# Kernel optimization log

Measured on AMD Instinct MI355X. Metric: run time of the kernel, lower is better.

## Reference

```python
import jax, jax.numpy as jnp
import numpy as np

D_MODEL = 1024
NUM_HEADS = 16
HEAD_DIM = D_MODEL // NUM_HEADS  # 64
SEQ = 2048
BATCH = 4
LN_EPS = 1e-5


def setup_inputs() -> dict:
    key = jax.random.key(0)
    k_in, k_qkv, k_o, k_g = jax.random.split(key, 4)
    inputs = jax.random.normal(k_in, (BATCH, SEQ, D_MODEL), dtype=jnp.float32)
    mask = jnp.zeros((BATCH, 1, SEQ, SEQ), dtype=jnp.float32)  # additive mask
    # Realistic rotary embeddings (RoPE), duplicated-halves layout
    inv_freq = 1.0 / (10000.0 ** (jnp.arange(0, HEAD_DIM, 2, dtype=jnp.float32) / HEAD_DIM))
    pos = jnp.arange(SEQ, dtype=jnp.float32)
    freqs = pos[:, None] * inv_freq[None, :]            # [S, Dh/2]
    emb = jnp.concatenate([freqs, freqs], axis=-1)       # [S, Dh]
    cos = jnp.cos(emb)
    sin = jnp.sin(emb)
    # Parameters
    sd = 1.0 / np.sqrt(D_MODEL)
    w_qkv = jax.random.normal(k_qkv, (D_MODEL, 3 * D_MODEL), dtype=jnp.float32) * sd
    w_o = jax.random.normal(k_o, (D_MODEL, D_MODEL), dtype=jnp.float32) * sd
    ln_gamma = jnp.ones((D_MODEL,), dtype=jnp.float32)
    return {"inputs": inputs, "mask": mask, "cos": cos, "sin": sin,
            "ln_gamma": ln_gamma, "w_qkv": w_qkv, "w_o": w_o}


def _rotate_half(x):
    x1, x2 = jnp.split(x, 2, axis=-1)
    return jnp.concatenate([-x2, x1], axis=-1)


def reference(inputs, mask, cos, sin, ln_gamma, w_qkv, w_o):
    B, S, D = inputs.shape
    # Pre-attention LayerNorm (layer_id != 0), center=False -> no beta
    mu = jnp.mean(inputs, axis=-1, keepdims=True)
    var = jnp.mean(jnp.square(inputs - mu), axis=-1, keepdims=True)
    x = (inputs - mu) / jnp.sqrt(var + LN_EPS) * ln_gamma
    # Fused QKV projection, split into heads: [B, H, S, Dh]
    qkv = (x @ w_qkv).reshape(B, S, 3, NUM_HEADS, HEAD_DIM)
    qkv = jnp.transpose(qkv, (2, 0, 3, 1, 4))
    q, k, v = qkv[0], qkv[1], qkv[2]
    # RoPE
    c = cos.reshape(1, 1, S, HEAD_DIM)
    s = sin.reshape(1, 1, S, HEAD_DIM)
    q = q * c + _rotate_half(q) * s
    k = k * c + _rotate_half(k) * s
    # Scaled dot-product attention with additive mask
    scale = 1.0 / jnp.sqrt(jnp.asarray(HEAD_DIM, dtype=q.dtype))
    logits = jnp.einsum("bhqd,bhkd->bhqk", q, k) * scale + mask
    attn = jax.nn.softmax(logits, axis=-1)
    out = jnp.einsum("bhqk,bhkd->bhqd", attn, v)
    out = jnp.transpose(out, (0, 2, 1, 3)).reshape(B, S, D)
    return out @ w_o
```

## Files before the change

kernel.cpp:

```cpp
#include <hip/hip_runtime.h>
#include <stdint.h>

#define DEV __device__ __forceinline__

typedef __bf16 bf16x8 __attribute__((ext_vector_type(8)));
typedef float f32x4 __attribute__((ext_vector_type(4)));
typedef float f32x16 __attribute__((ext_vector_type(16)));

DEV unsigned short f2bf(float f) {
  union { float f; uint32_t u; } c; c.f = f;
  uint32_t u = c.u;
  u += 0x7FFFu + ((u >> 16) & 1u);
  return (unsigned short)(u >> 16);
}
DEV float bf2f(unsigned short h) {
  union { uint32_t u; float f; } c; c.u = ((uint32_t)h) << 16;
  return c.f;
}
DEV float u2f(uint32_t u) {
  union { uint32_t u; float f; } c; c.u = u;
  return c.f;
}
DEV bf16x8 ld8(const unsigned short* p) {
  uint4 u = *reinterpret_cast<const uint4*>(p);
  return __builtin_bit_cast(bf16x8, u);
}
DEV uint32_t cvtpk(float lo, float hi) {
  uint32_t r;
  asm("v_cvt_pk_bf16_f32 %0, %1, %2" : "=v"(r) : "v"(lo), "v"(hi));
  return r;
}
DEV void permswap(uint32_t& a, uint32_t& b) {
  asm("v_permlane32_swap_b32 %0, %1" : "+v"(a), "+v"(b));
}
DEV float exp2b(float x) { return __builtin_amdgcn_exp2f(x); }
DEV void gload16(const void* g, void* l) {
  __builtin_amdgcn_global_load_lds((const __attribute__((address_space(1))) void*)g,
                                   (__attribute__((address_space(3))) void*)l, 16, 0, 0);
}

template<int K, int N>
__global__ __launch_bounds__(256)
void transpose_cast_kernel(const float* __restrict__ in, unsigned short* __restrict__ out) {
  __shared__ float tile[64][65];
  const int bk = blockIdx.x % (K / 64);
  const int bn = blockIdx.x / (K / 64);
  const int k0 = bk * 64, n0 = bn * 64;
  const int t = threadIdx.x;
#pragma unroll
  for (int i = 0; i < 16; ++i) {
    int idx = t + i * 256;
    int kl = idx >> 6, nl = idx & 63;
    tile[kl][nl] = in[(size_t)(k0 + kl) * N + n0 + nl];
  }
  __syncthreads();
#pragma unroll
  for (int i = 0; i < 16; ++i) {
    int idx = t + i * 256;
    int nl = idx >> 6, kl = idx & 63;
    out[(size_t)(n0 + nl) * K + k0 + kl] = f2bf(tile[kl][nl]);
  }
}

__global__ __launch_bounds__(256)
void ln_kernel(const float* __restrict__ x, const float* __restrict__ gamma,
               unsigned short* __restrict__ y) {
  const int row = blockIdx.x;
  const int t = threadIdx.x;
  const float4 v = reinterpret_cast<const float4*>(x + (size_t)row * 1024)[t];
  float s  = v.x + v.y + v.z + v.w;
  float s2 = v.x * v.x + v.y * v.y + v.z * v.z + v.w * v.w;
#pragma unroll
  for (int off = 1; off < 64; off <<= 1) {
    s  += __shfl_xor(s, off);
    s2 += __shfl_xor(s2, off);
  }
  __shared__ float red[8];
  const int w = t >> 6, lane = t & 63;
  if (lane == 0) { red[w] = s; red[4 + w] = s2; }
  __syncthreads();
  s  = red[0] + red[1] + red[2] + red[3];
  s2 = red[4] + red[5] + red[6] + red[7];
  const float mu = s * (1.0f / 1024.0f);
  const float var = s2 * (1.0f / 1024.0f) - mu * mu;
  const float rstd = rsqrtf(var + 1e-5f);
  const float4 g = reinterpret_cast<const float4*>(gamma)[t];
  ushort4 o;
  o.x = f2bf((v.x - mu) * rstd * g.x);
  o.y = f2bf((v.y - mu) * rstd * g.y);
  o.z = f2bf((v.z - mu) * rstd * g.z);
  o.w = f2bf((v.w - mu) * rstd * g.w);
  reinterpret_cast<ushort4*>(y + (size_t)row * 1024)[t] = o;
}

template<int N_DIM, bool OUT_F32>
__global__ __launch_bounds__(256)
void gemm_bt_kernel(const unsigned short* __restrict__ A,
                    const unsigned short* __restrict__ Bt,
                    void* __restrict__ Cout) {
  constexpr int K = 1024;
  __shared__ unsigned short a_lds[128 * 32];
  __shared__ unsigned short b_lds[128 * 32];
  const int t = threadIdx.x;
  const int w = t >> 6, l = t & 63;
  const int lrow = l & 15, lch = l >> 4;
  const int nbn = N_DIM / 128;
  const int m0 = (blockIdx.x / nbn) * 128;
  const int n0 = (blockIdx.x % nbn) * 128;
  const int wm = (w >> 1) * 64, wn = (w & 1) * 64;

  const int srow = t >> 2;
  const int schk = t & 3;
  const int scol = ((schk ^ (srow & 3)) << 3);
  const unsigned short* aS0 = A  + (size_t)(m0 + srow) * K + scol;
  const unsigned short* aS1 = A  + (size_t)(m0 + 64 + srow) * K + scol;
  const unsigned short* bS0 = Bt + (size_t)(n0 + srow) * K + scol;
  const unsigned short* bS1 = Bt + (size_t)(n0 + 64 + srow) * K + scol;
  unsigned short* aD0 = a_lds + (w * 16) * 32;
  unsigned short* aD1 = a_lds + (64 + w * 16) * 32;
  unsigned short* bD0 = b_lds + (w * 16) * 32;
  unsigned short* bD1 = b_lds + (64 + w * 16) * 32;

  f32x4 acc[4][4] = {};

  for (int k0 = 0; k0 < K; k0 += 32) {
    gload16(aS0 + k0, aD0);
    gload16(aS1 + k0, aD1);
    gload16(bS0 + k0, bD0);
    gload16(bS1 + k0, bD1);
    __syncthreads();
    bf16x8 af[4], bfr[4];
#pragma unroll
    for (int m = 0; m < 4; ++m) {
      int row = wm + m * 16 + lrow;
      af[m] = ld8(a_lds + row * 32 + ((lch ^ (lrow & 3)) << 3));
    }
#pragma unroll
    for (int n = 0; n < 4; ++n) {
      int row = wn + n * 16 + lrow;
      bfr[n] = ld8(b_lds + row * 32 + ((lch ^ (lrow & 3)) << 3));
    }
#pragma unroll
    for (int m = 0; m < 4; ++m)
#pragma unroll
      for (int n = 0; n < 4; ++n)
        acc[m][n] = __builtin_amdgcn_mfma_f32_16x16x32_bf16(af[m], bfr[n], acc[m][n], 0, 0, 0);
    __syncthreads();
  }

#pragma unroll
  for (int m = 0; m < 4; ++m) {
    const int grow0 = m0 + wm + m * 16 + lch * 4;
#pragma unroll
    for (int n = 0; n < 4; ++n) {
      const int gcol = n0 + wn + n * 16 + lrow;
#pragma unroll
      for (int r = 0; r < 4; ++r) {
        if constexpr (OUT_F32)
          ((float*)Cout)[(size_t)(grow0 + r) * N_DIM + gcol] = acc[m][n][r];
        else
          ((unsigned short*)Cout)[(size_t)(grow0 + r) * N_DIM + gcol] = f2bf(acc[m][n][r]);
      }
    }
  }
}

__global__ __launch_bounds__(256)
void rope_split_kernel(const unsigned short* __restrict__ qkv,
                       const float* __restrict__ cosb,
                       const float* __restrict__ sinb,
                       unsigned short* __restrict__ Qo,
                       unsigned short* __restrict__ Ko,
                       unsigned short* __restrict__ Vo) {
  const int bid = blockIdx.x;
  const int sb = bid & 31, h = (bid >> 5) & 15, b = bid >> 9;
  const int s0 = sb * 64;
  const int t = threadIdx.x;
  __shared__ unsigned short qt[64][72], kt[64][72], vt[64][72];

  const int sl = t >> 2, c0 = (t & 3) * 16;
  {
    const size_t base = (size_t)(b * 2048 + s0 + sl) * 3072 + h * 64 + c0;
    uint4 q1 = *(const uint4*)(qkv + base);
    uint4 q2 = *(const uint4*)(qkv + base + 8);
    uint4 k1 = *(const uint4*)(qkv + base + 1024);
    uint4 k2 = *(const uint4*)(qkv + base + 1032);
    uint4 v1 = *(const uint4*)(qkv + base + 2048);
    uint4 v2 = *(const uint4*)(qkv + base + 2056);
    *(uint4*)&qt[sl][c0] = q1; *(uint4*)&qt[sl][c0 + 8] = q2;
    *(uint4*)&kt[sl][c0] = k1; *(uint4*)&kt[sl][c0 + 8] = k2;
    *(uint4*)&vt[sl][c0] = v1; *(uint4*)&vt[sl][c0 + 8] = v2;
  }
  __syncthreads();
  {
    const int sg = s0 + sl;
    alignas(16) unsigned short qo16[16], ko16[16];
#pragma unroll
    for (int j = 0; j < 16; ++j) {
      const int d = c0 + j;
      const float cv = cosb[sg * 64 + d], sv = sinb[sg * 64 + d];
      const float qv = bf2f(qt[sl][d]), qp = bf2f(qt[sl][d ^ 32]);
      const float kv = bf2f(kt[sl][d]), kp = bf2f(kt[sl][d ^ 32]);
      const float rq = qv * cv + ((d < 32) ? -qp : qp) * sv;
      const float rk = kv * cv + ((d < 32) ? -kp : kp) * sv;
      qo16[j] = f2bf(rq * 0.180336880f);
      ko16[j] = f2bf(rk);
    }
    const size_t ob = ((size_t)(b * 16 + h) * 2048 + sg) * 64 + c0;
    *(uint4*)(Qo + ob) = *(uint4*)qo16; *(uint4*)(Qo + ob + 8) = *(uint4*)(qo16 + 8);
    *(uint4*)(Ko + ob) = *(uint4*)ko16; *(uint4*)(Ko + ob + 8) = *(uint4*)(ko16 + 8);
  }
  {
    const int dh = t >> 2, sc0 = (t & 3) * 16;
    alignas(16) unsigned short vo16[16];
#pragma unroll
    for (int j = 0; j < 16; ++j) vo16[j] = vt[sc0 + j][dh];
    const size_t ob = ((size_t)(b * 16 + h) * 64 + dh) * 2048 + s0 + sc0;
    *(uint4*)(Vo + ob) = *(uint4*)vo16; *(uint4*)(Vo + ob + 8) = *(uint4*)(vo16 + 8);
  }
}

__global__ __launch_bounds__(256)
void mask_flags_kernel(const float* __restrict__ mask, unsigned char* __restrict__ flg) {
  const int bid = blockIdx.x;
  const int kvt = bid & 31, qc = (bid >> 5) & 31, b = bid >> 10;
  const int t = threadIdx.x;
  uint32_t orbits = 0;
  const int r = t >> 2, c0 = (t & 3) * 16;
  const float* src = mask + (size_t)b * (2048ull * 2048) + (size_t)(qc * 64 + r) * 2048 + kvt * 64 + c0;
#pragma unroll
  for (int i = 0; i < 4; ++i) {
    const float4 v = *(const float4*)(src + i * 4);
    orbits |= __float_as_uint(v.x) | __float_as_uint(v.y) |
              __float_as_uint(v.z) | __float_as_uint(v.w);
  }
  const int nz = __syncthreads_or(orbits != 0u);
  if (t == 0) flg[(size_t)(b * 32 + kvt) * 32 + qc] = (unsigned char)(nz != 0);
}

__global__ __launch_bounds__(256)
void mask_retile_kernel(const float* __restrict__ mask, unsigned short* __restrict__ mrs,
                        const unsigned char* __restrict__ flg) {
  const int bid = blockIdx.x;
  const int kvt = bid & 31, qc = (bid >> 5) & 31, b = bid >> 10;
  if (!flg[(size_t)(b * 32 + kvt) * 32 + qc]) return;
  const int t = threadIdx.x;
  __shared__ float tile[64][72];
  {
    const int r = t >> 2, c0 = (t & 3) * 16;
    const float* src = mask + (size_t)b * (2048ull * 2048) + (size_t)(qc * 64 + r) * 2048 + kvt * 64 + c0;
#pragma unroll
    for (int i = 0; i < 4; ++i) {
      const float4 v = *(const float4*)(src + i * 4);
      *(float4*)&tile[r][c0 + i * 4] = v;
    }
  }
  __syncthreads();
  const int cid = t >> 5;
  const int n = cid >> 2, jj = (cid >> 1) & 1, hi = cid & 1;
  const int qq0 = (t & 31) * 2;
  const int cb = n * 32 + jj * 16 + hi * 4;
  unsigned short* dst = mrs + (((size_t)(b * 32 + kvt) * 8 + cid) * 2048 + qc * 64) * 8;
#pragma unroll
  for (int qo = 0; qo < 2; ++qo) {
    const int q = qq0 + qo;
    alignas(16) unsigned short o8[8];
#pragma unroll
    for (int v = 0; v < 8; ++v) {
      const int col = cb + (v >> 2) * 8 + (v & 3);
      o8[v] = f2bf(tile[q][col] * 1.44269504f);
    }
    *(uint4*)(dst + (size_t)q * 8) = *(uint4*)o8;
  }
}

__global__ __launch_bounds__(256)
void attn_kernel(const unsigned short* __restrict__ Q,
                 const unsigned short* __restrict__ Kg,
                 const unsigned short* __restrict__ Vt,
                 const unsigned short* __restrict__ mrs,
                 const unsigned char* __restrict__ flg,
                 unsigned short* __restrict__ O) {
  const int t = threadIdx.x, w = t >> 6, l = t & 63;
  const int lq = l & 31, hi = l >> 5;
  const int bid = blockIdx.x;
  const int x = bid & 7, y = bid >> 3;
  const int bh = x * 8 + (y & 7), qb = y >> 3;
  const int b = bh >> 4, h = bh & 15;
  const int q0 = qb * 128 + w * 32;

  const unsigned short* Qb = Q  + (size_t)bh * (2048 * 64);
  const unsigned short* Kb = Kg + (size_t)bh * (2048 * 64);
  const unsigned short* Vb = Vt + (size_t)bh * (64 * 2048);
  const unsigned short* ml = mrs + (size_t)b * 4194304 + (size_t)hi * 16384 + (size_t)(q0 + lq) * 8;
  const unsigned char* fb = flg + (size_t)(b * 32) * 32 + qb * 2;

  __shared__ unsigned short k_lds[2][64 * 64];
  __shared__ unsigned short v_lds[2][64 * 64];

  bf16x8 qf[4];
  {
    const unsigned short* qp = Qb + (size_t)(q0 + lq) * 64 + hi * 8;
#pragma unroll
    for (int c = 0; c < 4; ++c) qf[c] = ld8(qp + c * 16);
  }
  bf16x8 ones;
  {
    const uint4 ou = { 0x3F803F80u, 0x3F803F80u, 0x3F803F80u, 0x3F803F80u };
    ones = __builtin_bit_cast(bf16x8, ou);
  }

  const int srow = t >> 2, sl0 = (t & 3) * 2, sl1 = sl0 + 1;
  const unsigned short* ks = Kb + (size_t)srow * 64 + sl0 * 8;
  const unsigned short* vs = Vb + (size_t)srow * 2048 + sl0 * 8;
  const int wd0 = srow * 64 + ((sl0 ^ (srow & 7)) << 3);
  const int wd1 = srow * 64 + ((sl1 ^ (srow & 7)) << 3);

  uint4 ka0 = *(const uint4*)ks;
  uint4 ka1 = *(const uint4*)(ks + 8);
  uint4 va0 = *(const uint4*)vs;
  uint4 va1 = *(const uint4*)(vs + 8);
  *(uint4*)(k_lds[0] + wd0) = ka0;
  *(uint4*)(k_lds[0] + wd1) = ka1;
  *(uint4*)(v_lds[0] + wd0) = va0;
  *(uint4*)(v_lds[0] + wd1) = va1;

  f32x16 ot0 = {}, ot1 = {};
  f32x16 st_sum = {};
  int cur = 0;
  const int lsw = lq & 7;

  uint4 mA[4], mB[4];

  auto do_tile = [&](int kv0, uint4 (&mcur)[4], uint4 (&mnext)[4],
                     bool hm, bool hmn) {
    __syncthreads();
    const bool more = (kv0 + 64) < 2048;
    if (more) {
      ka0 = *(const uint4*)(ks + (size_t)(kv0 + 64) * 64);
      ka1 = *(const uint4*)(ks + (size_t)(kv0 + 64) * 64 + 8);
      va0 = *(const uint4*)(vs + kv0 + 64);
      va1 = *(const uint4*)(vs + kv0 + 64 + 8);
      if (hmn) {
        const unsigned short* mp = ml + (size_t)(kv0 + 64) * 2048;
#pragma unroll
        for (int c2 = 0; c2 < 4; ++c2) mnext[c2] = *(const uint4*)(mp + c2 * 32768);
      }
    }

    f32x16 st0 = {}, st1 = {};
    if (hm) {
#pragma unroll
      for (int jj = 0; jj < 2; ++jj) {
        const uint4 u0 = mcur[jj];
        const uint4 u1 = mcur[2 + jj];
#pragma unroll
        for (int wv = 0; wv < 4; ++wv) {
          const uint32_t w0 = ((const uint32_t*)&u0)[wv];
          const uint32_t w1 = ((const uint32_t*)&u1)[wv];
          st0[jj * 8 + wv * 2]     = u2f(w0 << 16);
          st0[jj * 8 + wv * 2 + 1] = u2f(w0 & 0xffff0000u);
          st1[jj * 8 + wv * 2]     = u2f(w1 << 16);
          st1[jj * 8 + wv * 2 + 1] = u2f(w1 & 0xffff0000u);
        }
      }
    }

    const unsigned short* kb = k_lds[cur];
    __builtin_amdgcn_s_setprio(1);
#pragma unroll
    for (int c = 0; c < 4; ++c) {
      const int so = (((2 * c + hi) ^ lsw) << 3);
      const bf16x8 kf0 = ld8(kb + lq * 64 + so);
      const bf16x8 kf1 = ld8(kb + (32 + lq) * 64 + so);
      st0 = __builtin_amdgcn_mfma_f32_32x32x16_bf16(kf0, qf[c], st0, 0, 0, 0);
      st1 = __builtin_amdgcn_mfma_f32_32x32x16_bf16(kf1, qf[c], st1, 0, 0, 0);
    }
    __builtin_amdgcn_s_setprio(0);

#pragma unroll
    for (int r = 0; r < 16; ++r) {
      st0[r] = exp2b(st0[r]);
      st1[r] = exp2b(st1[r]);
    }

    bf16x8 pa[4];
#pragma unroll
    for (int c = 0; c < 4; ++c) {
      const int e8 = (c & 1) * 8;
      uint32_t A01, B01, A23, B23;
      if (c < 2) {
        A01 = cvtpk(st0[e8 + 0], st0[e8 + 1]);
        B01 = cvtpk(st0[e8 + 4], st0[e8 + 5]);
        A23 = cvtpk(st0[e8 + 2], st0[e8 + 3]);
        B23 = cvtpk(st0[e8 + 6], st0[e8 + 7]);
      } else {
        A01 = cvtpk(st1[e8 + 0], st1[e8 + 1]);
        B01 = cvtpk(st1[e8 + 4], st1[e8 + 5]);
        A23 = cvtpk(st1[e8 + 2], st1[e8 + 3]);
        B23 = cvtpk(st1[e8 + 6], st1[e8 + 7]);
      }
      permswap(A01, B01);
      permswap(A23, B23);
      const uint4 pw = { A01, A23, B01, B23 };
      pa[c] = __builtin_bit_cast(bf16x8, pw);
    }

    if (more) {
      unsigned short* kn = k_lds[cur ^ 1];
      unsigned short* vn = v_lds[cur ^ 1];
      *(uint4*)(kn + wd0) = ka0;
      *(uint4*)(kn + wd1) = ka1;
      *(uint4*)(vn + wd0) = va0;
      *(uint4*)(vn + wd1) = va1;
    }

    const unsigned short* vb = v_lds[cur];
    __builtin_amdgcn_s_setprio(1);
#pragma unroll
    for (int c = 0; c < 4; ++c) {
      const int so = (((2 * c + hi) ^ lsw) << 3);
      const bf16x8 vf0 = ld8(vb + lq * 64 + so);
      const bf16x8 vf1 = ld8(vb + (32 + lq) * 64 + so);
      ot0 = __builtin_amdgcn_mfma_f32_32x32x16_bf16(vf0, pa[c], ot0, 0, 0, 0);
      ot1 = __builtin_amdgcn_mfma_f32_32x32x16_bf16(vf1, pa[c], ot1, 0, 0, 0);
      st_sum = __builtin_amdgcn_mfma_f32_32x32x16_bf16(ones, pa[c], st_sum, 0, 0, 0);
    }
    __builtin_amdgcn_s_setprio(0);
    cur ^= 1;
  };

  unsigned int bm = 0;
  for (int kvt = 0; kvt < 32; ++kvt) bm |= fb[kvt * 32] | fb[kvt * 32 + 1];

  if (bm == 0) {
    for (int kv0 = 0; kv0 < 2048; kv0 += 128) {
      do_tile(kv0, mA, mB, false, false);
      do_tile(kv0 + 64, mB, mA, false, false);
    }
  } else {
    bool hmA = (fb[0] | fb[1]) != 0;
    if (hmA) {
#pragma unroll
      for (int c2 = 0; c2 < 4; ++c2) mA[c2] = *(const uint4*)(ml + c2 * 32768);
    }
    bool hmB = false;
    for (int kv0 = 0; kv0 < 2048; kv0 += 128) {
      const int tB = (kv0 >> 6) + 1;
      hmB = (kv0 + 64 < 2048) && ((fb[tB * 32] | fb[tB * 32 + 1]) != 0);
      do_tile(kv0, mA, mB, hmA, hmB);
      const int tA = tB + 1;
      hmA = (kv0 + 128 < 2048) && ((fb[tA * 32] | fb[tA * 32 + 1]) != 0);
      do_tile(kv0 + 64, mB, mA, hmB, hmA);
    }
  }

  const float inv = 1.0f / st_sum[0];
  unsigned short* ob = O + ((size_t)(b * 2048 + q0 + lq) * 16 + h) * 64 + hi * 4;
#pragma unroll
  for (int td = 0; td < 2; ++td) {
#pragma unroll
    for (int rr = 0; rr < 4; ++rr) {
      ushort4 ov;
      if (td == 0) {
        ov.x = f2bf(ot0[rr * 4 + 0] * inv);
        ov.y = f2bf(ot0[rr * 4 + 1] * inv);
        ov.z = f2bf(ot0[rr * 4 + 2] * inv);
        ov.w = f2bf(ot0[rr * 4 + 3] * inv);
      } else {
        ov.x = f2bf(ot1[rr * 4 + 0] * inv);
        ov.y = f2bf(ot1[rr * 4 + 1] * inv);
        ov.z = f2bf(ot1[rr * 4 + 2] * inv);
        ov.w = f2bf(ot1[rr * 4 + 3] * inv);
      }
      *(ushort4*)(ob + td * 32 + rr * 8) = ov;
    }
  }
}

extern "C" void kernel_launch(void* const* d_in, const int* in_sizes, int n_in,
                              void* d_out, int out_size, void* d_ws, size_t ws_size,
                              hipStream_t stream) {
  (void)in_sizes; (void)n_in; (void)out_size; (void)ws_size;
  const float* x     = (const float*)d_in[0];
  const float* mask  = (const float*)d_in[1];
  const float* cosb  = (const float*)d_in[2];
  const float* sinb  = (const float*)d_in[3];
  const float* gamma = (const float*)d_in[4];
  const float* w_qkv = (const float*)d_in[5];
  const float* w_o   = (const float*)d_in[6];

  char* ws = (char*)d_ws;
  unsigned short* x_bf   = (unsigned short*)(ws);
  unsigned short* wqkvT  = (unsigned short*)(ws + 16777216);
  unsigned short* woT    = (unsigned short*)(ws + 23068672);
  unsigned short* qkv_bf = (unsigned short*)(ws + 25165824);
  unsigned short* q_r    = (unsigned short*)(ws + 75497472);
  unsigned short* k_r    = (unsigned short*)(ws + 92274688);
  unsigned short* v_t    = (unsigned short*)(ws + 109051904);
  unsigned short* attn   = (unsigned short*)(ws + 125829120);
  unsigned short* mask_rs = qkv_bf;
  unsigned char*  flags   = (unsigned char*)(ws + 25165824 + 33554432);

  transpose_cast_kernel<1024, 3072><<<dim3(16 * 48), dim3(256), 0, stream>>>(w_qkv, wqkvT);
  transpose_cast_kernel<1024, 1024><<<dim3(16 * 16), dim3(256), 0, stream>>>(w_o, woT);
  ln_kernel<<<dim3(8192), dim3(256), 0, stream>>>(x, gamma, x_bf);
  gemm_bt_kernel<3072, false><<<dim3(64 * 24), dim3(256), 0, stream>>>(x_bf, wqkvT, (void*)qkv_bf);
  rope_split_kernel<<<dim3(4 * 16 * 32), dim3(256), 0, stream>>>(qkv_bf, cosb, sinb, q_r, k_r, v_t);
  mask_flags_kernel<<<dim3(4096), dim3(256), 0, stream>>>(mask, flags);
  mask_retile_kernel<<<dim3(4096), dim3(256), 0, stream>>>(mask, mask_rs, flags);
  attn_kernel<<<dim3(1024), dim3(256), 0, stream>>>(q_r, k_r, v_t, mask_rs, flags, attn);
  gemm_bt_kernel<1024, true><<<dim3(64 * 8), dim3(256), 0, stream>>>(attn, woT, d_out);
}
```

Before: 241.6 us.

## Fuse RoPE, head split and V transpose into QKV GEMM epilogue

The separate rope_split kernel is removed. The QKV GEMM epilogue now applies RoPE and the Q scale, and writes Q/K in head-major layout and V transposed directly from the MFMA accumulators. This avoids writing and re-reading the full bf16 QKV intermediate and saves one launch. In exchange the epilogue does scattered 2-byte stores and per-element cos/sin loads, which coalesce less well than the old staged writes.

```diff
diff --git a/kernel.cpp b/kernel.cpp
--- a/kernel.cpp
+++ b/kernel.cpp
@@ -93,11 +93,11 @@
   reinterpret_cast<ushort4*>(y + (size_t)row * 1024)[t] = o;
 }
 
-template<int N_DIM, bool OUT_F32>
+template<int N_DIM>
 __global__ __launch_bounds__(256)
 void gemm_bt_kernel(const unsigned short* __restrict__ A,
                     const unsigned short* __restrict__ Bt,
-                    void* __restrict__ Cout) {
+                    float* __restrict__ Cout) {
   constexpr int K = 1024;
   __shared__ unsigned short a_lds[128 * 32];
   __shared__ unsigned short b_lds[128 * 32];
@@ -155,68 +155,114 @@
     for (int n = 0; n < 4; ++n) {
       const int gcol = n0 + wn + n * 16 + lrow;
 #pragma unroll
+      for (int r = 0; r < 4; ++r)
+        Cout[(size_t)(grow0 + r) * N_DIM + gcol] = acc[m][n][r];
+    }
+  }
+}
+
+__global__ __launch_bounds__(256)
+void gemm_qkv_rope_kernel(const unsigned short* __restrict__ A,
+                          const unsigned short* __restrict__ Bt,
+                          const float* __restrict__ cosb,
+                          const float* __restrict__ sinb,
+                          unsigned short* __restrict__ Qo,
+                          unsigned short* __restrict__ Ko,
+                          unsigned short* __restrict__ Vo) {
+  constexpr int K = 1024;
+  constexpr int N_DIM = 3072;
+  __shared__ unsigned short a_lds[128 * 32];
+  __shared__ unsigned short b_lds[128 * 32];
+  const int t = threadIdx.x;
+  const int w = t >> 6, l = t & 63;
+  const int lrow = l & 15, lch = l >> 4;
+  const int nbn = N_DIM / 128;
+  const int m0 = (blockIdx.x / nbn) * 128;
+  const int n0 = (blockIdx.x % nbn) * 128;
+  const int wm = (w >> 1) * 64, wn = (w & 1) * 64;
+
+  const int srow = t >> 2;
+  const int schk = t & 3;
+  const int scol = ((schk ^ (srow & 3)) << 3);
+  const unsigned short* aS0 = A  + (size_t)(m0 + srow) * K + scol;
+  const unsigned short* aS1 = A  + (size_t)(m0 + 64 + srow) * K + scol;
+  const unsigned short* bS0 = Bt + (size_t)(n0 + srow) * K + scol;
+  const unsigned short* bS1 = Bt + (size_t)(n0 + 64 + srow) * K + scol;
+  unsigned short* aD0 = a_lds + (w * 16) * 32;
+  unsigned short* aD1 = a_lds + (64 + w * 16) * 32;
+  unsigned short* bD0 = b_lds + (w * 16) * 32;
+  unsigned short* bD1 = b_lds + (64 + w * 16) * 32;
+
+  f32x4 acc[4][4] = {};
+
+  for (int k0 = 0; k0 < K; k0 += 32) {
+    gload16(aS0 + k0, aD0);
+    gload16(aS1 + k0, aD1);
+    gload16(bS0 + k0, bD0);
+    gload16(bS1 + k0, bD1);
+    __syncthreads();
+    bf16x8 af[4], bfr[4];
+#pragma unroll
+    for (int m = 0; m < 4; ++m) {
+      int row = wm + m * 16 + lrow;
+      af[m] = ld8(a_lds + row * 32 + ((lch ^ (lrow & 3)) << 3));
+    }
+#pragma unroll
+    for (int n = 0; n < 4; ++n) {
+      int row = wn + n * 16 + lrow;
+      bfr[n] = ld8(b_lds + row * 32 + ((lch ^ (lrow & 3)) << 3));
+    }
+#pragma unroll
+    for (int m = 0; m < 4; ++m)
+#pragma unroll
+      for (int n = 0; n < 4; ++n)
+        acc[m][n] = __builtin_amdgcn_mfma_f32_16x16x32_bf16(af[m], bfr[n], acc[m][n], 0, 0, 0);
+    __syncthreads();
+  }
+
+  const int b = m0 >> 11;
+  const int sbase = (m0 & 2047) + wm;
+  const int region = n0 >> 10;
+  const int h = ((n0 & 1023) >> 6) + (w & 1);
+
+  if (region < 2) {
+    const float qs = (region == 0) ? 0.180336880f : 1.0f;
+    unsigned short* dst = (region == 0 ? Qo : Ko) + (size_t)(b * 16 + h) * 2048 * 64;
+#pragma unroll
+    for (int m = 0; m < 4; ++m) {
+#pragma unroll
       for (int r = 0; r < 4; ++r) {
-        if constexpr (OUT_F32)
-          ((float*)Cout)[(size_t)(grow0 + r) * N_DIM + gcol] = acc[m][n][r];
-        else
-          ((unsigned short*)Cout)[(size_t)(grow0 + r) * N_DIM + gcol] = f2bf(acc[m][n][r]);
+        const int sg = sbase + m * 16 + lch * 4 + r;
+        const float* crow = cosb + (size_t)sg * 64;
+        const float* srow2 = sinb + (size_t)sg * 64;
+        unsigned short* drow = dst + (size_t)sg * 64;
+#pragma unroll
+        for (int np = 0; np < 2; ++np) {
+          const int d0 = np * 16 + lrow;
+          const int d1 = d0 + 32;
+          const float v0 = acc[m][np][r];
+          const float v1 = acc[m][np + 2][r];
+          const float r0 = v0 * crow[d0] - v1 * srow2[d0];
+          const float r1 = v1 * crow[d1] + v0 * srow2[d1];
+          drow[d0] = f2bf(r0 * qs);
+          drow[d1] = f2bf(r1 * qs);
+        }
       }
     }
-  }
-}
-
-__global__ __launch_bounds__(256)
-void rope_split_kernel(const unsigned short* __restrict__ qkv,
-                       const float* __restrict__ cosb,
-                       const float* __restrict__ sinb,
-                       unsigned short* __restrict__ Qo,
-                       unsigned short* __restrict__ Ko,
-                       unsigned short* __restrict__ Vo) {
-  const int bid = blockIdx.x;
-  const int sb = bid & 31, h = (bid >> 5) & 15, b = bid >> 9;
-  const int s0 = sb * 64;
-  const int t = threadIdx.x;
-  __shared__ unsigned short qt[64][72], kt[64][72], vt[64][72];
-
-  const int sl = t >> 2, c0 = (t & 3) * 16;
-  {
-    const size_t base = (size_t)(b * 2048 + s0 + sl) * 3072 + h * 64 + c0;
-    uint4 q1 = *(const uint4*)(qkv + base);
-    uint4 q2 = *(const uint4*)(qkv + base + 8);
-    uint4 k1 = *(const uint4*)(qkv + base + 1024);
-    uint4 k2 = *(const uint4*)(qkv + base + 1032);
-    uint4 v1 = *(const uint4*)(qkv + base + 2048);
-    uint4 v2 = *(const uint4*)(qkv + base + 2056);
-    *(uint4*)&qt[sl][c0] = q1; *(uint4*)&qt[sl][c0 + 8] = q2;
-    *(uint4*)&kt[sl][c0] = k1; *(uint4*)&kt[sl][c0 + 8] = k2;
-    *(uint4*)&vt[sl][c0] = v1; *(uint4*)&vt[sl][c0 + 8] = v2;
-  }
-  __syncthreads();
-  {
-    const int sg = s0 + sl;
-    alignas(16) unsigned short qo16[16], ko16[16];
-#pragma unroll
-    for (int j = 0; j < 16; ++j) {
-      const int d = c0 + j;
-      const float cv = cosb[sg * 64 + d], sv = sinb[sg * 64 + d];
-      const float qv = bf2f(qt[sl][d]), qp = bf2f(qt[sl][d ^ 32]);
-      const float kv = bf2f(kt[sl][d]), kp = bf2f(kt[sl][d ^ 32]);
-      const float rq = qv * cv + ((d < 32) ? -qp : qp) * sv;
-      const float rk = kv * cv + ((d < 32) ? -kp : kp) * sv;
-      qo16[j] = f2bf(rq * 0.180336880f);
-      ko16[j] = f2bf(rk);
-    }
-    const size_t ob = ((size_t)(b * 16 + h) * 2048 + sg) * 64 + c0;
-    *(uint4*)(Qo + ob) = *(uint4*)qo16; *(uint4*)(Qo + ob + 8) = *(uint4*)(qo16 + 8);
-    *(uint4*)(Ko + ob) = *(uint4*)ko16; *(uint4*)(Ko + ob + 8) = *(uint4*)(ko16 + 8);
-  }
-  {
-    const int dh = t >> 2, sc0 = (t & 3) * 16;
-    alignas(16) unsigned short vo16[16];
-#pragma unroll
-    for (int j = 0; j < 16; ++j) vo16[j] = vt[sc0 + j][dh];
-    const size_t ob = ((size_t)(b * 16 + h) * 64 + dh) * 2048 + s0 + sc0;
-    *(uint4*)(Vo + ob) = *(uint4*)vo16; *(uint4*)(Vo + ob + 8) = *(uint4*)(vo16 + 8);
+  } else {
+    unsigned short* dst = Vo + (size_t)(b * 16 + h) * 64 * 2048;
+#pragma unroll
+    for (int m = 0; m < 4; ++m) {
+      const int sg0 = sbase + m * 16 + lch * 4;
+#pragma unroll
+      for (int np = 0; np < 4; ++np) {
+        const int d = np * 16 + lrow;
+        alignas(8) unsigned short o4[4];
+#pragma unroll
+        for (int r = 0; r < 4; ++r) o4[r] = f2bf(acc[m][np][r]);
+        *(ushort4*)(dst + (size_t)d * 2048 + sg0) = *(ushort4*)o4;
+      }
+    }
   }
 }
 
@@ -494,21 +540,19 @@
   unsigned short* x_bf   = (unsigned short*)(ws);
   unsigned short* wqkvT  = (unsigned short*)(ws + 16777216);
   unsigned short* woT    = (unsigned short*)(ws + 23068672);
-  unsigned short* qkv_bf = (unsigned short*)(ws + 25165824);
+  unsigned short* mask_rs = (unsigned short*)(ws + 25165824);
+  unsigned char*  flags   = (unsigned char*)(ws + 25165824 + 33554432);
   unsigned short* q_r    = (unsigned short*)(ws + 75497472);
   unsigned short* k_r    = (unsigned short*)(ws + 92274688);
   unsigned short* v_t    = (unsigned short*)(ws + 109051904);
   unsigned short* attn   = (unsigned short*)(ws + 125829120);
-  unsigned short* mask_rs = qkv_bf;
-  unsigned char*  flags   = (unsigned char*)(ws + 25165824 + 33554432);
 
   transpose_cast_kernel<1024, 3072><<<dim3(16 * 48), dim3(256), 0, stream>>>(w_qkv, wqkvT);
   transpose_cast_kernel<1024, 1024><<<dim3(16 * 16), dim3(256), 0, stream>>>(w_o, woT);
   ln_kernel<<<dim3(8192), dim3(256), 0, stream>>>(x, gamma, x_bf);
-  gemm_bt_kernel<3072, false><<<dim3(64 * 24), dim3(256), 0, stream>>>(x_bf, wqkvT, (void*)qkv_bf);
-  rope_split_kernel<<<dim3(4 * 16 * 32), dim3(256), 0, stream>>>(qkv_bf, cosb, sinb, q_r, k_r, v_t);
+  gemm_qkv_rope_kernel<<<dim3(64 * 24), dim3(256), 0, stream>>>(x_bf, wqkvT, cosb, sinb, q_r, k_r, v_t);
   mask_flags_kernel<<<dim3(4096), dim3(256), 0, stream>>>(mask, flags);
   mask_retile_kernel<<<dim3(4096), dim3(256), 0, stream>>>(mask, mask_rs, flags);
   attn_kernel<<<dim3(1024), dim3(256), 0, stream>>>(q_r, k_r, v_t, mask_rs, flags, attn);
-  gemm_bt_kernel<1024, true><<<dim3(64 * 8), dim3(256), 0, stream>>>(attn, woT, d_out);
-}
+  gemm_bt_kernel<1024><<<dim3(64 * 8), dim3(256), 0, stream>>>(attn, woT, (float*)d_out);
+}
```

Result: faster. 233.2 us (-3.5%).
